# Performance work log

Hardware: AMD Instinct MI355X
Metric: run time of the kernel (lower is better)

Reference implementation:

```python
import jax, jax.numpy as jnp
import numpy as np


def setup_inputs() -> dict:
    key = jax.random.key(0)
    k1, k2, k3 = jax.random.split(key, 3)
    B, E, L, D = 32, 256, 2048, 256
    doc_state = jax.random.normal(k1, (B, L, D), dtype=jnp.float32)
    entity_mapping = jax.random.uniform(k2, (B, E, L), dtype=jnp.float32)
    entity_lens = jax.random.uniform(k3, (B, E), dtype=jnp.float32)
    return {"doc_state": doc_state, "entity_mapping": entity_mapping, "entity_lens": entity_lens}


def reference(doc_state, entity_mapping, entity_lens):
    # Original: (entity_mapping[:, :, :, None] * doc_state[:, None, :, :]).sum(2) / entity_lens[:, :, None]
    # This is a batched contraction over L; express as einsum to avoid the
    # huge [B, E, L, D] intermediate.
    summed = jnp.einsum('bel,bld->bed', entity_mapping, doc_state)  # [B, E, D]
    return summed / entity_lens[:, :, None]
```

## Files before the change

### kernel.cpp

```cpp
#include <hip/hip_runtime.h>
#include <stdint.h>

#define B_ 32
#define E_ 256
#define L_ 2048
#define D_ 256

#define BE 64
#define BD 128
#define BK 64
#define KS 4
#define KCHUNK (L_ / KS)
#define NKT (KCHUNK / BK)

typedef __attribute__((ext_vector_type(2))) float  f32x2;
typedef __attribute__((ext_vector_type(4))) float  f32x4;
typedef __attribute__((ext_vector_type(4))) short  s16x4;
typedef __attribute__((ext_vector_type(8))) short  s16x8;

__device__ __forceinline__ void cvt_hilo1(float x, short &h, short &l) {
    unsigned u = __builtin_bit_cast(unsigned, x);
    h = (short)(u >> 16);
    float hf = __builtin_bit_cast(float, u & 0xFFFF0000u);
    unsigned r = __builtin_bit_cast(unsigned, x - hf);
    l = (short)(r >> 16);
}
__device__ __forceinline__ void cvt_hilo4(const f32x4 v, s16x4 &h, s16x4 &l) {
    #pragma unroll
    for (int i = 0; i < 4; ++i) { short hh, ll; cvt_hilo1(v[i], hh, ll); h[i] = hh; l[i] = ll; }
}

__global__ void zero_out_kernel(f32x4* __restrict__ out) {
    out[(size_t)blockIdx.x * 256 + threadIdx.x] = f32x4{0.f, 0.f, 0.f, 0.f};
}

__global__ __launch_bounds__(512, 6)
void mean_pool_kernel(const float* __restrict__ doc,
                      const float* __restrict__ emap,
                      const float* __restrict__ lens,
                      float* __restrict__ out) {
    __shared__ __align__(16) short As_hi[BE][BK];
    __shared__ __align__(16) short As_lo[BE][BK];
    __shared__ __align__(16) short Bs_hi[BD][BK];
    __shared__ __align__(16) short Bs_lo[BD][BK];
    __shared__ float lens_s[BE];

    const int t   = threadIdx.x;
    const int blk = blockIdx.x;
    const int ks  = blk & 3;
    const int d0  = ((blk >> 2) & 1) * BD;
    const int e0  = ((blk >> 3) & 3) * BE;
    const int b   = blk >> 5;

    const float* Ag = emap + ((size_t)b * E_ + e0) * L_ + ks * KCHUNK;
    const float* Sg = doc  + (size_t)b * L_ * D_ + (size_t)ks * KCHUNK * D_ + d0;

    if (t < BE) lens_s[t] = lens[b * E_ + e0 + t];

    const int a_c4 = t & 15;
    const int a_r  = t >> 4;
    const int db = t & 63;
    const int kb = t >> 6;

    const int lane = t & 63;
    const int w    = t >> 6;
    const int eo   = (w & 1) * 32;
    const int dq   = (w >> 1) * 32;
    const int ml   = lane & 15;
    const int kg   = lane >> 4;

    f32x4 acc[2][2] = {};
    f32x4 pa[2];
    f32x2 pb[8];

    #pragma unroll
    for (int rr = 0; rr < 2; ++rr)
        pa[rr] = *(const f32x4*)(Ag + (size_t)(a_r + rr * 32) * L_ + a_c4 * 4);
    #pragma unroll
    for (int i = 0; i < 8; ++i)
        pb[i] = *(const f32x2*)(Sg + (size_t)(kb * 8 + i) * D_ + db * 2);

    for (int kt = 0; kt < NKT; ++kt) {
        #pragma unroll
        for (int rr = 0; rr < 2; ++rr) {
            const int row = a_r + rr * 32;
            s16x4 h, l;
            cvt_hilo4(pa[rr], h, l);
            const int col = (((a_c4 >> 1) ^ (row & 7)) << 3) + (a_c4 & 1) * 4;
            *(s16x4*)&As_hi[row][col] = h;
            *(s16x4*)&As_lo[row][col] = l;
        }
        #pragma unroll
        for (int dd = 0; dd < 2; ++dd) {
            const int row = db * 2 + dd;
            s16x8 h, l;
            #pragma unroll
            for (int j = 0; j < 8; ++j) {
                short hh, ll; cvt_hilo1(pb[j][dd], hh, ll);
                h[j] = hh; l[j] = ll;
            }
            const int key = (db & 3) | (((db >> 2) & 1) << 2);
            const int col = (kb ^ key) << 3;
            *(s16x8*)&Bs_hi[row][col] = h;
            *(s16x8*)&Bs_lo[row][col] = l;
        }
        __syncthreads();

        if (kt + 1 < NKT) {
            const int k0 = (kt + 1) * BK;
            #pragma unroll
            for (int rr = 0; rr < 2; ++rr)
                pa[rr] = *(const f32x4*)(Ag + (size_t)(a_r + rr * 32) * L_ + k0 + a_c4 * 4);
            #pragma unroll
            for (int i = 0; i < 8; ++i)
                pb[i] = *(const f32x2*)(Sg + (size_t)(k0 + kb * 8 + i) * D_ + db * 2);
        }

        #pragma unroll
        for (int kc = 0; kc < 2; ++kc) {
            const int gbase = kc * 4;
            s16x8 ah[2], al[2], bh[2], bl[2];
            #pragma unroll
            for (int mi = 0; mi < 2; ++mi) {
                const int row = eo + mi * 16 + ml;
                const int col = ((gbase + kg) ^ (row & 7)) << 3;
                ah[mi] = *(const s16x8*)&As_hi[row][col];
                al[mi] = *(const s16x8*)&As_lo[row][col];
            }
            #pragma unroll
            for (int ni = 0; ni < 2; ++ni) {
                const int row = dq + ni * 16 + ml;
                const int keyB = ((row >> 1) & 3) | (((row >> 3) & 1) << 2);
                const int col  = ((gbase + kg) ^ keyB) << 3;
                bh[ni] = *(const s16x8*)&Bs_hi[row][col];
                bl[ni] = *(const s16x8*)&Bs_lo[row][col];
            }
            #pragma unroll
            for (int mi = 0; mi < 2; ++mi)
                #pragma unroll
                for (int ni = 0; ni < 2; ++ni) {
                    acc[mi][ni] = __builtin_amdgcn_mfma_f32_16x16x32_bf16(ah[mi], bh[ni], acc[mi][ni], 0, 0, 0);
                    acc[mi][ni] = __builtin_amdgcn_mfma_f32_16x16x32_bf16(ah[mi], bl[ni], acc[mi][ni], 0, 0, 0);
                    acc[mi][ni] = __builtin_amdgcn_mfma_f32_16x16x32_bf16(al[mi], bh[ni], acc[mi][ni], 0, 0, 0);
                }
        }
        __syncthreads();
    }

    #pragma unroll
    for (int mi = 0; mi < 2; ++mi) {
        #pragma unroll
        for (int rr = 0; rr < 4; ++rr) {
            const int er = eo + mi * 16 + kg * 4 + rr;
            const float lv = lens_s[er];
            #pragma unroll
            for (int ni = 0; ni < 2; ++ni) {
                atomicAdd(&out[((size_t)(b * E_ + e0 + er)) * D_ + d0 + dq + ni * 16 + ml],
                          acc[mi][ni][rr] / lv);
            }
        }
    }
}

extern "C" void kernel_launch(void* const* d_in, const int* in_sizes, int n_in,
                              void* d_out, int out_size, void* d_ws, size_t ws_size,
                              hipStream_t stream) {
    const float* doc  = (const float*)d_in[0];
    const float* emap = (const float*)d_in[1];
    const float* lens = (const float*)d_in[2];
    float* out = (float*)d_out;

    zero_out_kernel<<<dim3(out_size / (4 * 256)), dim3(256), 0, stream>>>((f32x4*)out);

    dim3 grid(B_ * (E_ / BE) * (D_ / BD) * KS);
    dim3 block(512);
    hipLaunchKernelGGL(mean_pool_kernel, grid, block, 0, stream,
                       doc, emap, lens, out);
}
```

Before: 174.1 us.

## Enlarge block tile to 128x256, double-buffer LDS, drop second barrier

Tiles grow from 64x128 to 128x256 per block with a smaller K step of 32, so each wave now computes a 64x64 output with 4x4 MFMA accumulators. LDS is double-buffered, which lets each K iteration drop its trailing barrier. Swizzled LDS offsets are precomputed once outside the loop, and s_setprio raises wave priority around the MFMA section. The larger tile means fewer redundant global reads of emap and doc, but it also means fewer blocks (256), higher register pressure, and lower occupancy (launch bounds 2).

```diff
diff --git a/kernel.cpp b/kernel.cpp
--- a/kernel.cpp
+++ b/kernel.cpp
@@ -6,9 +6,9 @@
 #define L_ 2048
 #define D_ 256
 
-#define BE 64
-#define BD 128
-#define BK 64
+#define BE 128
+#define BD 256
+#define BK 32
 #define KS 4
 #define KCHUNK (L_ / KS)
 #define NKT (KCHUNK / BK)
@@ -18,6 +18,9 @@
 typedef __attribute__((ext_vector_type(4))) short  s16x4;
 typedef __attribute__((ext_vector_type(8))) short  s16x8;
 
+#define KEYA(row) ((((row) >> 1) & 3) | (((row) & 1) << 2))
+#define KEYB(row) (((row) >> 1) & 7)
+
 __device__ __forceinline__ void cvt_hilo1(float x, short &h, short &l) {
     unsigned u = __builtin_bit_cast(unsigned, x);
     h = (short)(u >> 16);
@@ -25,84 +28,99 @@
     unsigned r = __builtin_bit_cast(unsigned, x - hf);
     l = (short)(r >> 16);
 }
-__device__ __forceinline__ void cvt_hilo4(const f32x4 v, s16x4 &h, s16x4 &l) {
-    #pragma unroll
-    for (int i = 0; i < 4; ++i) { short hh, ll; cvt_hilo1(v[i], hh, ll); h[i] = hh; l[i] = ll; }
-}
 
 __global__ void zero_out_kernel(f32x4* __restrict__ out) {
     out[(size_t)blockIdx.x * 256 + threadIdx.x] = f32x4{0.f, 0.f, 0.f, 0.f};
 }
 
-__global__ __launch_bounds__(512, 6)
+__global__ __launch_bounds__(512, 2)
 void mean_pool_kernel(const float* __restrict__ doc,
                       const float* __restrict__ emap,
                       const float* __restrict__ lens,
                       float* __restrict__ out) {
-    __shared__ __align__(16) short As_hi[BE][BK];
-    __shared__ __align__(16) short As_lo[BE][BK];
-    __shared__ __align__(16) short Bs_hi[BD][BK];
-    __shared__ __align__(16) short Bs_lo[BD][BK];
+    __shared__ __align__(16) short As[2][BE][64];
+    __shared__ __align__(16) short Bs[2][BD][64];
     __shared__ float lens_s[BE];
 
     const int t   = threadIdx.x;
     const int blk = blockIdx.x;
     const int ks  = blk & 3;
-    const int d0  = ((blk >> 2) & 1) * BD;
-    const int e0  = ((blk >> 3) & 3) * BE;
-    const int b   = blk >> 5;
+    const int e0  = ((blk >> 2) & 1) * BE;
+    const int b   = blk >> 3;
 
     const float* Ag = emap + ((size_t)b * E_ + e0) * L_ + ks * KCHUNK;
-    const float* Sg = doc  + (size_t)b * L_ * D_ + (size_t)ks * KCHUNK * D_ + d0;
+    const float* Sg = doc  + (size_t)b * L_ * D_ + (size_t)ks * KCHUNK * D_;
 
     if (t < BE) lens_s[t] = lens[b * E_ + e0 + t];
 
-    const int a_c4 = t & 15;
-    const int a_r  = t >> 4;
-    const int db = t & 63;
-    const int kb = t >> 6;
+    const int a_c4 = t & 7;
+    const int a_r  = t >> 3;
+    const int dp   = t & 127;
+    const int kb   = t >> 7;
 
     const int lane = t & 63;
     const int w    = t >> 6;
-    const int eo   = (w & 1) * 32;
-    const int dq   = (w >> 1) * 32;
+    const int eo   = (w & 1) * 64;
+    const int dq   = (w >> 1) * 64;
     const int ml   = lane & 15;
     const int kg   = lane >> 4;
 
-    f32x4 acc[2][2] = {};
+    int awo_h[2], awo_l[2];
+    #pragma unroll
+    for (int rr = 0; rr < 2; ++rr) {
+        const int row = a_r + rr * 64, k = KEYA(row), hb = (a_c4 & 1) * 4;
+        awo_h[rr] = row * 64 + ((((a_c4 >> 1)    ) ^ k) << 3) + hb;
+        awo_l[rr] = row * 64 + ((((a_c4 >> 1) | 4) ^ k) << 3) + hb;
+    }
+    int bwo_h[2], bwo_l[2];
+    #pragma unroll
+    for (int dd = 0; dd < 2; ++dd) {
+        const int row = dp * 2 + dd, k = KEYB(row);
+        bwo_h[dd] = row * 64 + (((kb    ) ^ k) << 3);
+        bwo_l[dd] = row * 64 + (((kb | 4) ^ k) << 3);
+    }
+    int aro_h[4], aro_l[4], bro_h[4], bro_l[4];
+    #pragma unroll
+    for (int i = 0; i < 4; ++i) {
+        const int ar = eo + i * 16 + ml, ka = KEYA(ar);
+        aro_h[i] = ar * 64 + (((kg    ) ^ ka) << 3);
+        aro_l[i] = ar * 64 + (((kg | 4) ^ ka) << 3);
+        const int br = dq + i * 16 + ml, kB = KEYB(br);
+        bro_h[i] = br * 64 + (((kg    ) ^ kB) << 3);
+        bro_l[i] = br * 64 + (((kg | 4) ^ kB) << 3);
+    }
+
+    f32x4 acc[4][4] = {};
     f32x4 pa[2];
     f32x2 pb[8];
 
     #pragma unroll
     for (int rr = 0; rr < 2; ++rr)
-        pa[rr] = *(const f32x4*)(Ag + (size_t)(a_r + rr * 32) * L_ + a_c4 * 4);
+        pa[rr] = *(const f32x4*)(Ag + (size_t)(a_r + rr * 64) * L_ + a_c4 * 4);
     #pragma unroll
-    for (int i = 0; i < 8; ++i)
-        pb[i] = *(const f32x2*)(Sg + (size_t)(kb * 8 + i) * D_ + db * 2);
+    for (int j = 0; j < 8; ++j)
+        pb[j] = *(const f32x2*)(Sg + (size_t)(kb * 8 + j) * D_ + dp * 2);
 
+    #pragma unroll 2
     for (int kt = 0; kt < NKT; ++kt) {
+        short* Ab = &As[kt & 1][0][0];
+        short* Bb = &Bs[kt & 1][0][0];
+
         #pragma unroll
         for (int rr = 0; rr < 2; ++rr) {
-            const int row = a_r + rr * 32;
             s16x4 h, l;
-            cvt_hilo4(pa[rr], h, l);
-            const int col = (((a_c4 >> 1) ^ (row & 7)) << 3) + (a_c4 & 1) * 4;
-            *(s16x4*)&As_hi[row][col] = h;
-            *(s16x4*)&As_lo[row][col] = l;
+            #pragma unroll
+            for (int i = 0; i < 4; ++i) { short hh, ll; cvt_hilo1(pa[rr][i], hh, ll); h[i] = hh; l[i] = ll; }
+            *(s16x4*)&Ab[awo_h[rr]] = h;
+            *(s16x4*)&Ab[awo_l[rr]] = l;
         }
         #pragma unroll
         for (int dd = 0; dd < 2; ++dd) {
-            const int row = db * 2 + dd;
             s16x8 h, l;
             #pragma unroll
-            for (int j = 0; j < 8; ++j) {
-                short hh, ll; cvt_hilo1(pb[j][dd], hh, ll);
-                h[j] = hh; l[j] = ll;
-            }
-            const int key = (db & 3) | (((db >> 2) & 1) << 2);
-            const int col = (kb ^ key) << 3;
-            *(s16x8*)&Bs_hi[row][col] = h;
-            *(s16x8*)&Bs_lo[row][col] = l;
+            for (int j = 0; j < 8; ++j) { short hh, ll; cvt_hilo1(pb[j][dd], hh, ll); h[j] = hh; l[j] = ll; }
+            *(s16x8*)&Bb[bwo_h[dd]] = h;
+            *(s16x8*)&Bb[bwo_l[dd]] = l;
         }
         __syncthreads();
 
@@ -110,54 +128,43 @@
             const int k0 = (kt + 1) * BK;
             #pragma unroll
             for (int rr = 0; rr < 2; ++rr)
-                pa[rr] = *(const f32x4*)(Ag + (size_t)(a_r + rr * 32) * L_ + k0 + a_c4 * 4);
+                pa[rr] = *(const f32x4*)(Ag + (size_t)(a_r + rr * 64) * L_ + k0 + a_c4 * 4);
             #pragma unroll
-            for (int i = 0; i < 8; ++i)
-                pb[i] = *(const f32x2*)(Sg + (size_t)(k0 + kb * 8 + i) * D_ + db * 2);
+            for (int j = 0; j < 8; ++j)
+                pb[j] = *(const f32x2*)(Sg + (size_t)(k0 + kb * 8 + j) * D_ + dp * 2);
         }
 
+        s16x8 bh[4], bl[4];
         #pragma unroll
-        for (int kc = 0; kc < 2; ++kc) {
-            const int gbase = kc * 4;
-            s16x8 ah[2], al[2], bh[2], bl[2];
+        for (int ni = 0; ni < 4; ++ni) {
+            bh[ni] = *(const s16x8*)&Bb[bro_h[ni]];
+            bl[ni] = *(const s16x8*)&Bb[bro_l[ni]];
+        }
+        __builtin_amdgcn_s_setprio(1);
+        #pragma unroll
+        for (int mi = 0; mi < 4; ++mi) {
+            const s16x8 ah = *(const s16x8*)&Ab[aro_h[mi]];
+            const s16x8 al = *(const s16x8*)&Ab[aro_l[mi]];
             #pragma unroll
-            for (int mi = 0; mi < 2; ++mi) {
-                const int row = eo + mi * 16 + ml;
-                const int col = ((gbase + kg) ^ (row & 7)) << 3;
-                ah[mi] = *(const s16x8*)&As_hi[row][col];
-                al[mi] = *(const s16x8*)&As_lo[row][col];
+            for (int ni = 0; ni < 4; ++ni) {
+                acc[mi][ni] = __builtin_amdgcn_mfma_f32_16x16x32_bf16(ah, bh[ni], acc[mi][ni], 0, 0, 0);
+                acc[mi][ni] = __builtin_amdgcn_mfma_f32_16x16x32_bf16(ah, bl[ni], acc[mi][ni], 0, 0, 0);
+                acc[mi][ni] = __builtin_amdgcn_mfma_f32_16x16x32_bf16(al, bh[ni], acc[mi][ni], 0, 0, 0);
             }
-            #pragma unroll
-            for (int ni = 0; ni < 2; ++ni) {
-                const int row = dq + ni * 16 + ml;
-                const int keyB = ((row >> 1) & 3) | (((row >> 3) & 1) << 2);
-                const int col  = ((gbase + kg) ^ keyB) << 3;
-                bh[ni] = *(const s16x8*)&Bs_hi[row][col];
-                bl[ni] = *(const s16x8*)&Bs_lo[row][col];
-            }
-            #pragma unroll
-            for (int mi = 0; mi < 2; ++mi)
-                #pragma unroll
-                for (int ni = 0; ni < 2; ++ni) {
-                    acc[mi][ni] = __builtin_amdgcn_mfma_f32_16x16x32_bf16(ah[mi], bh[ni], acc[mi][ni], 0, 0, 0);
-                    acc[mi][ni] = __builtin_amdgcn_mfma_f32_16x16x32_bf16(ah[mi], bl[ni], acc[mi][ni], 0, 0, 0);
-                    acc[mi][ni] = __builtin_amdgcn_mfma_f32_16x16x32_bf16(al[mi], bh[ni], acc[mi][ni], 0, 0, 0);
-                }
         }
-        __syncthreads();
+        __builtin_amdgcn_s_setprio(0);
     }
 
     #pragma unroll
-    for (int mi = 0; mi < 2; ++mi) {
+    for (int mi = 0; mi < 4; ++mi) {
         #pragma unroll
         for (int rr = 0; rr < 4; ++rr) {
             const int er = eo + mi * 16 + kg * 4 + rr;
             const float lv = lens_s[er];
             #pragma unroll
-            for (int ni = 0; ni < 2; ++ni) {
-                atomicAdd(&out[((size_t)(b * E_ + e0 + er)) * D_ + d0 + dq + ni * 16 + ml],
+            for (int ni = 0; ni < 4; ++ni)
+                atomicAdd(&out[((size_t)(b * E_ + e0 + er)) * D_ + dq + ni * 16 + ml],
                           acc[mi][ni][rr] / lv);
-            }
         }
     }
 }
```

Result: slower. 177.9 us (+2.1%).
